# Kernel tuning notes

Hardware: AMD Instinct MI355X
Metric: run time of the kernel (lower is better)

Reference implementation:

```python
import jax, jax.numpy as jnp
import numpy as np

TEMPERATURE = 0.8
TOP_K = 50
TOP_P = 0.9
REP_PENALTY = 1.2
NEG_INF = -1000000000.0


def setup_inputs() -> dict:
    key = jax.random.key(0)
    k1, k2 = jax.random.split(key)
    B, S, V, L = 64, 8, 50257, 2048
    logits = jax.random.normal(k1, (B, S, V), dtype=jnp.float32)
    input_ids = jax.random.randint(k2, (B, L), 0, V, dtype=jnp.int64)
    return {"logits": logits, "input_ids": input_ids}


def _modify_logits(logits, input_ids):
    B, S, V = logits.shape
    # temperature scale
    x = logits / TEMPERATURE
    # top-k: keep values >= k-th largest (ties negligible for random floats)
    kth = jax.lax.top_k(x, TOP_K)[0][..., -1:]  # [B,S,1]
    x = jnp.where(x >= kth, x, NEG_INF)
    # top-p nucleus filtering
    order = jnp.argsort(-x, axis=-1)                       # descending order indices
    sorted_logits = jnp.take_along_axis(x, order, axis=-1)
    cum = jnp.cumsum(jax.nn.softmax(sorted_logits, axis=-1), axis=-1)
    remove = cum > TOP_P
    # shift right by one; always keep the top token
    remove = jnp.concatenate([jnp.zeros_like(remove[..., :1]), remove[..., :-1]], axis=-1)
    inv = jnp.argsort(order, axis=-1)                      # inverse permutation
    remove_orig = jnp.take_along_axis(remove, inv, axis=-1)
    x = jnp.where(remove_orig, NEG_INF, x)
    # repetition penalty on last position only, for tokens present in history
    present = jnp.zeros((B, V), dtype=bool).at[
        jnp.arange(B)[:, None], input_ids
    ].set(True)
    last = x[:, -1, :]
    penalized = jnp.where(last < 0, last * REP_PENALTY, last / REP_PENALTY)
    last = jnp.where(present, penalized, last)
    return x.at[:, -1, :].set(last)


def reference(logits, input_ids):
    return _modify_logits(logits, input_ids)
```

## Files before the change

kernel.cpp:

```cpp
#include <hip/hip_runtime.h>
#include <stdint.h>

#define V 50257
#define B_ 64
#define S_ 8
#define ROWS (B_ * S_)
#define L_ 2048
#define NEG_INF -1000000000.0f
#define PEN_NEG (-1200000000.0f)
#define MASK_WORDS_PER_B 1571
#define TOTAL (ROWS * V)
#define NVEC (TOTAL / 4)
#define TOP_CAP 64
#define TRAW 2.8f
#define GBLK_F4 1571
#define GBLOCKS_G ((NVEC + GBLK_F4 - 1) / GBLK_F4)
#define GCAP_BLK 64
#define CAPROW 512
#define NPRESW ((GBLK_F4 * 4 + 31) / 32)

#define WS_BCNT    0
#define WS_GCAND   16384
#define WS_NEED    (WS_GCAND + (size_t)GBLOCKS_G * GCAP_BLK * 8)
#define WS_ROWPARAM 0
#define WS_MASK     8192

__device__ __forceinline__ unsigned fkey(float f) {
    unsigned u = __float_as_uint(f);
    return (u & 0x80000000u) ? ~u : (u | 0x80000000u);
}

__device__ __forceinline__ int blockReduceSum256(int v, int tid, int* s4) {
#pragma unroll
    for (int off = 32; off; off >>= 1) v += __shfl_down(v, off);
    __syncthreads();
    if ((tid & 63) == 0) s4[tid >> 6] = v;
    __syncthreads();
    return s4[0] + s4[1] + s4[2] + s4[3];
}


__global__ __launch_bounds__(256) void prep_kernel(const float4* __restrict__ in4,
                                                   const int* __restrict__ ids,
                                                   float4* __restrict__ out4,
                                                   uint2* __restrict__ gcand,
                                                   unsigned* __restrict__ bcnt) {
    const int blk = blockIdx.x;
    const int tid = threadIdx.x;
    const int start = blk * GBLK_F4;
    const int end = min(start + GBLK_F4, NVEC);
    const unsigned baseE = (unsigned)start << 2;
    const unsigned endE = (unsigned)end << 2;

    __shared__ unsigned pres[NPRESW];
    __shared__ uint2 buf[GCAP_BLK];
    __shared__ int lcnt;

    for (int w = tid; w < NPRESW; w += 256) pres[w] = 0u;
    if (tid == 0) lcnt = 0;
    {
        unsigned r0 = baseE / (unsigned)V, r1 = (endE - 1u) / (unsigned)V;
        unsigned rl = ((r0 & 7u) == 7u) ? r0 : (((r1 & 7u) == 7u) ? r1 : 0xFFFFFFFFu);
        if (rl != 0xFFFFFFFFu) {
            __syncthreads();
            const int* bp = ids + (rl >> 3) * L_;
            unsigned rowBase = rl * (unsigned)V;
#pragma unroll
            for (int k = 0; k < L_ / 256; ++k) {
                unsigned ge = rowBase + (unsigned)bp[k * 256 + tid];
                if (ge >= baseE && ge < endE) {
                    unsigned off = ge - baseE;
                    atomicOr(&pres[off >> 5], 1u << (off & 31));
                }
            }
        }
    }
    __syncthreads();

    float4 va0 = in4[min(start + tid,            NVEC - 1)];
    float4 va1 = in4[min(start + tid + 256,      NVEC - 1)];
    float4 va2 = in4[min(start + tid + 2 * 256,  NVEC - 1)];
    float4 va3 = in4[min(start + tid + 3 * 256,  NVEC - 1)];
    float4 va4 = in4[min(start + tid + 4 * 256,  NVEC - 1)];
    float4 va5 = in4[min(start + tid + 5 * 256,  NVEC - 1)];
    float4 va6 = in4[min(start + tid + 6 * 256,  NVEC - 1)];
    __builtin_amdgcn_sched_barrier(0);
    float4 va[7] = {va0, va1, va2, va3, va4, va5, va6};
#pragma unroll
    for (int k = 0; k < 7; ++k) {
        int i = start + tid + k * 256;
        if (i < end) {
            float4 a = va[k];
            unsigned e = (unsigned)i << 2;
            if (a.x >= TRAW) { int p = atomicAdd(&lcnt, 1); if (p < GCAP_BLK) buf[p] = make_uint2(e,      __float_as_uint(a.x)); }
            if (a.y >= TRAW) { int p = atomicAdd(&lcnt, 1); if (p < GCAP_BLK) buf[p] = make_uint2(e + 1u, __float_as_uint(a.y)); }
            if (a.z >= TRAW) { int p = atomicAdd(&lcnt, 1); if (p < GCAP_BLK) buf[p] = make_uint2(e + 2u, __float_as_uint(a.z)); }
            if (a.w >= TRAW) { int p = atomicAdd(&lcnt, 1); if (p < GCAP_BLK) buf[p] = make_uint2(e + 3u, __float_as_uint(a.w)); }
            unsigned off = e - baseE;
            unsigned pw = pres[off >> 5] >> (off & 31u);
            float4 bg;
            bg.x = (pw & 1u) ? PEN_NEG : NEG_INF;
            bg.y = (pw & 2u) ? PEN_NEG : NEG_INF;
            bg.z = (pw & 4u) ? PEN_NEG : NEG_INF;
            bg.w = (pw & 8u) ? PEN_NEG : NEG_INF;
            out4[i] = bg;
        }
    }

    __syncthreads();
    if (tid == 0) bcnt[blk] = (unsigned)lcnt;
    int take = min(lcnt, GCAP_BLK);
    for (int j = tid; j < take; j += 256) gcand[(size_t)blk * GCAP_BLK + j] = buf[j];
}


__global__ __launch_bounds__(256) void select_kernel(const float* __restrict__ logits,
                                                     const int* __restrict__ ids,
                                                     const uint2* __restrict__ gcand,
                                                     const unsigned* __restrict__ bcnt,
                                                     float* __restrict__ out) {
    const int row = blockIdx.x;
    const int tid = threadIdx.x;
    __shared__ float cX[CAPROW];
    __shared__ unsigned cR[CAPROW];
    __shared__ int cI[CAPROW];
    __shared__ float sVal[TOP_CAP];
    __shared__ int sIdx[TOP_CAP];
    __shared__ double sExp[TOP_CAP];
    __shared__ unsigned presRow[MASK_WORDS_PER_B];
    __shared__ int s_c, s_M, s_bad, s_ti;
    __shared__ float s_t;
    __shared__ int s_red[4];

    const float* rp = logits + (size_t)row * V;
    const unsigned e0 = (unsigned)row * (unsigned)V;
    if (tid == 0) { s_c = 0; s_bad = 0; }
    __syncthreads();

    {
        const int b0 = (int)((e0 >> 2) / GBLK_F4);
        const int b1 = (int)(((e0 + V - 1) >> 2) / GBLK_F4);
        for (int blk = b0; blk <= b1; ++blk) {
            unsigned c = bcnt[blk];
            if (c > GCAP_BLK && tid == 0) s_bad = 1;
            int take = min((int)c, GCAP_BLK);
            for (int j = tid; j < take; j += 256) {
                uint2 u = gcand[(size_t)blk * GCAP_BLK + j];
                if (u.x / (unsigned)V == (unsigned)row) {
                    int p = atomicAdd(&s_c, 1);
                    if (p < CAPROW) {
                        cR[p] = u.y;
                        cX[p] = __uint_as_float(u.y) / 0.8f;
                        cI[p] = (int)(u.x - e0);
                    }
                }
            }
        }
    }
    __syncthreads();
    int cnt = s_c;
    if (s_bad || cnt < 50 || cnt > CAPROW) {
        unsigned lo = 0u, hi = 0xFFFFFFFFu;
        while (lo < hi) {
            unsigned mid = lo + ((hi - lo) >> 1) + 1u;
            int c = 0;
            for (int j = tid; j < V; j += 256) c += (int)(fkey(rp[j]) >= mid);
            c = blockReduceSum256(c, tid, s_red);
            if (c >= 50) lo = mid; else hi = mid - 1u;
        }
        unsigned gl = (lo > 2u) ? lo - 2u : 0u;
        __syncthreads();
        if (tid == 0) s_c = 0;
        __syncthreads();
        for (int j = tid; j < V; j += 256) {
            float v = rp[j];
            if (fkey(v) >= gl) {
                int p = atomicAdd(&s_c, 1);
                if (p < CAPROW) { cR[p] = __float_as_uint(v); cX[p] = v / 0.8f; cI[p] = j; }
            }
        }
        __syncthreads();
        cnt = min(s_c, CAPROW);
    }

    if (tid < TOP_CAP) { sVal[tid] = -3.4e38f; sIdx[tid] = 0x7FFFFFFF; }
    __syncthreads();

    {
        float v0 = -3.4e38f, v1 = -3.4e38f;
        int i0 = 0x7FFFFFFF, i1 = 0x7FFFFFFF;
        if (tid < cnt) { v0 = cX[tid]; i0 = cI[tid]; }
        if (tid + 256 < cnt) { v1 = cX[tid + 256]; i1 = cI[tid + 256]; }
        int r0 = 0, r1 = 0;
        for (int j = 0; j < cnt; ++j) {
            float w = cX[j];
            int wi = cI[j];
            r0 += (w > v0) || (w == v0 && wi < i0);
            r1 += (w > v1) || (w == v1 && wi < i1);
        }
        if (tid < cnt && r0 < TOP_CAP) { sVal[r0] = v0; sIdx[r0] = i0; }
        if (tid + 256 < cnt && r1 < TOP_CAP) { sVal[r1] = v1; sIdx[r1] = i1; }
    }
    __syncthreads();

    if (tid == 0) {
        float kth = sVal[49];
        int M = 50;
        while (M < TOP_CAP && sVal[M] == kth) ++M;
        s_M = M;
    }
    __syncthreads();
    int M = s_M;
    if (tid < M) sExp[tid] = exp((double)sVal[tid] - (double)sVal[0]);
    __syncthreads();
    if (tid == 0) {
        double denom = 0.0;
        for (int i = 0; i < M; ++i) denom += sExp[i];
        double cum = 0.0;
        int J = M - 1;
        for (int i = 0; i < M; ++i) {
            cum += sExp[i] / denom;
            if (cum > 0.9) { J = i; break; }
        }
        s_t = sVal[J];
        s_ti = sIdx[J];
    }

    if ((row & 7) == 7) {
        __syncthreads();
        for (int w = tid; w < MASK_WORDS_PER_B; w += 256) presRow[w] = 0u;
        __syncthreads();
        const int* bp = ids + (row >> 3) * L_;
#pragma unroll
        for (int k = 0; k < L_ / 256; ++k) {
            int t = bp[k * 256 + tid];
            atomicOr(&presRow[t >> 5], 1u << (t & 31));
        }
    }
    __syncthreads();

    float t = s_t;
    int tie = s_ti;
    float* orow = out + (size_t)row * V;
    const bool pen = (row & 7) == 7;
    for (int j = tid; j < cnt; j += 256) {
        float x = cX[j];
        int tok = cI[j];
        bool keep = (x > t) || (x == t && tok <= tie);
        if (keep) {
            float oo = x;
            if (pen && ((presRow[tok >> 5] >> (tok & 31)) & 1u))
                oo = (oo < 0.0f) ? oo * 1.2f : oo * (1.0f / 1.2f);
            orow[tok] = oo;
        }
    }
}

#define CAND_CAP 4096
#define RT_THREADS 1024

__global__ __launch_bounds__(256) void mask_only_kernel(const int* __restrict__ ids,
                                                        unsigned* __restrict__ mask) {
    const int tid = threadIdx.x;
    const int b = blockIdx.x;
    __shared__ unsigned lds[MASK_WORDS_PER_B];
    for (int w = tid; w < MASK_WORDS_PER_B; w += 256) lds[w] = 0u;
    __syncthreads();
    const int* bp = ids + b * L_;
#pragma unroll
    for (int k = 0; k < L_ / 256; ++k) {
        int t = bp[k * 256 + tid];
        atomicOr(&lds[t >> 5], 1u << (t & 31));
    }
    __syncthreads();
    unsigned* mp = mask + b * MASK_WORDS_PER_B;
    for (int w = tid; w < MASK_WORDS_PER_B; w += 256) mp[w] = lds[w];
}

__global__ __launch_bounds__(RT_THREADS, 8) void row_thresh_kernel(
        const float* __restrict__ logits, uint4* __restrict__ rowParam) {
    const int tid = threadIdx.x;
    const int row = blockIdx.x;
    if (row >= ROWS) return;
    const float* rp = logits + (size_t)row * V;

    __shared__ float candV[CAND_CAP];
    __shared__ int   candI[CAND_CAP];
    __shared__ float sVal[TOP_CAP];
    __shared__ int   sIdx[TOP_CAP];
    __shared__ double sExp[TOP_CAP];
    __shared__ int s_cnt, s_M;
    __shared__ int s_red[RT_THREADS / 64];

    const unsigned mis = (unsigned)(((size_t)row * (size_t)V) & 3u);
    const int a0 = (int)((4u - mis) & 3u);
    const int nv = (V - a0) >> 2;
    const int tailStart = a0 + (nv << 2);
    const float4* vp = reinterpret_cast<const float4*>(rp + a0);

    float TR = 2.4f;
    int cnt = 0;
    for (int attempt = 0; attempt < 12; ++attempt) {
        if (tid == 0) s_cnt = 0;
        __syncthreads();
        for (int base = tid; base < nv; base += 4 * RT_THREADS) {
            int i1 = base + RT_THREADS, i2 = base + 2 * RT_THREADS, i3 = base + 3 * RT_THREADS;
            float4 a = vp[base];
            float4 b = vp[i1 < nv ? i1 : nv - 1];
            float4 c = vp[i2 < nv ? i2 : nv - 1];
            float4 d = vp[i3 < nv ? i3 : nv - 1];
            float va[16] = {a.x, a.y, a.z, a.w, b.x, b.y, b.z, b.w,
                            c.x, c.y, c.z, c.w, d.x, d.y, d.z, d.w};
            int ib[4] = {base, i1, i2, i3};
            bool ok[4] = {true, i1 < nv, i2 < nv, i3 < nv};
#pragma unroll
            for (int q = 0; q < 4; ++q) {
                if (!ok[q]) continue;
#pragma unroll
                for (int cc = 0; cc < 4; ++cc) {
                    float v = va[q * 4 + cc];
                    if (v >= TR) {
                        int p = atomicAdd(&s_cnt, 1);
                        if (p < CAND_CAP) { candV[p] = v / 0.8f; candI[p] = a0 + (ib[q] << 2) + cc; }
                    }
                }
            }
        }
        if (tid < a0) {
            float v = rp[tid];
            if (v >= TR) {
                int p = atomicAdd(&s_cnt, 1);
                if (p < CAND_CAP) { candV[p] = v / 0.8f; candI[p] = tid; }
            }
        }
        if (tid < V - tailStart) {
            float v = rp[tailStart + tid];
            if (v >= TR) {
                int p = atomicAdd(&s_cnt, 1);
                if (p < CAND_CAP) { candV[p] = v / 0.8f; candI[p] = tailStart + tid; }
            }
        }
        __syncthreads();
        cnt = s_cnt;
        if (cnt >= 50 && cnt <= CAND_CAP) break;
        if (cnt < 50) TR -= 1.2f; else TR += 1.2f;
        __syncthreads();
    }
    if (cnt > CAND_CAP) cnt = CAND_CAP;

    if (tid < TOP_CAP) { sVal[tid] = -3.4e38f; sIdx[tid] = 0x7FFFFFFF; }
    __syncthreads();

    {
        float v0 = (tid < cnt) ? candV[tid] : -3.4e38f;
        int i0 = (tid < cnt) ? candI[tid] : 0x7FFFFFFF;
        float v1 = (tid + RT_THREADS < cnt) ? candV[tid + RT_THREADS] : -3.4e38f;
        int i1 = (tid + RT_THREADS < cnt) ? candI[tid + RT_THREADS] : 0x7FFFFFFF;
        float v2 = (tid + 2 * RT_THREADS < cnt) ? candV[tid + 2 * RT_THREADS] : -3.4e38f;
        int i2 = (tid + 2 * RT_THREADS < cnt) ? candI[tid + 2 * RT_THREADS] : 0x7FFFFFFF;
        float v3 = (tid + 3 * RT_THREADS < cnt) ? candV[tid + 3 * RT_THREADS] : -3.4e38f;
        int i3 = (tid + 3 * RT_THREADS < cnt) ? candI[tid + 3 * RT_THREADS] : 0x7FFFFFFF;
        int r0 = 0, r1 = 0, r2 = 0, r3 = 0;
        for (int j = 0; j < cnt; ++j) {
            float w = candV[j];
            int wi = candI[j];
            r0 += (w > v0) || (w == v0 && wi < i0);
            r1 += (w > v1) || (w == v1 && wi < i1);
            r2 += (w > v2) || (w == v2 && wi < i2);
            r3 += (w > v3) || (w == v3 && wi < i3);
        }
        if (tid < cnt && r0 < TOP_CAP) { sVal[r0] = v0; sIdx[r0] = i0; }
        if (tid + RT_THREADS < cnt && r1 < TOP_CAP) { sVal[r1] = v1; sIdx[r1] = i1; }
        if (tid + 2 * RT_THREADS < cnt && r2 < TOP_CAP) { sVal[r2] = v2; sIdx[r2] = i2; }
        if (tid + 3 * RT_THREADS < cnt && r3 < TOP_CAP) { sVal[r3] = v3; sIdx[r3] = i3; }
    }
    __syncthreads();

    if (tid == 0) {
        float kth = sVal[49];
        int M = 50;
        while (M < TOP_CAP && sVal[M] == kth) ++M;
        s_M = M;
    }
    __syncthreads();
    int M = s_M;
    if (tid < M) sExp[tid] = exp((double)sVal[tid] - (double)sVal[0]);
    __syncthreads();

    if (tid == 0) {
        double denom = 0.0;
#pragma unroll 1
        for (int i = 0; i < M; ++i) denom += sExp[i];
        double cum = 0.0;
        int J = M - 1;
#pragma unroll 1
        for (int i = 0; i < M; ++i) {
            cum += sExp[i] / denom;
            if (cum > 0.9) { J = i; break; }
        }
        float t = sVal[J];
        float w = t * 0.8f;
        unsigned wb = __float_as_uint(w);
        unsigned lo = 0xFFFFFFFFu, hi = 0u;
        for (int d = -4; d <= 4; ++d) {
            unsigned ub = wb + (unsigned)d;
            if (__uint_as_float(ub) / 0.8f == t) { if (ub < lo) lo = ub; if (ub > hi) hi = ub; }
        }
        rowParam[row] = make_uint4(lo, hi, (unsigned)sIdx[J], 0u);
    }
}

__global__ __launch_bounds__(256) void apply_kernel(const float4* __restrict__ in4,
                                                    const uint4* __restrict__ rowParam,
                                                    const unsigned* __restrict__ mask,
                                                    float4* __restrict__ out4) {
    int gid = blockIdx.x * 256 + threadIdx.x;
    int i0 = gid << 1;
    if (i0 >= NVEC) return;
    float4 a = in4[i0];
    float4 b = in4[i0 + 1];
    unsigned e = (unsigned)i0 << 2;
    unsigned row = e / (unsigned)V;
    unsigned tok0 = e - row * (unsigned)V;
    uint4 p0 = rowParam[row];
    bool crosses = (tok0 + 7u >= (unsigned)V);
    uint4 p1 = crosses ? rowParam[row + 1] : p0;
    float xs[8] = {a.x, a.y, a.z, a.w, b.x, b.y, b.z, b.w};
    float o[8];
#pragma unroll
    for (int c = 0; c < 8; ++c) {
        unsigned tok = tok0 + (unsigned)c;
        unsigned r = row;
        uint4 pp = p0;
        if (tok >= (unsigned)V) { tok -= (unsigned)V; r = row + 1u; pp = p1; }
        float v = xs[c];
        float vlo = __uint_as_float(pp.x);
        float vhi = __uint_as_float(pp.y);
        bool keep = (v > vhi) || (v >= vlo && tok <= pp.z);
        float oo = keep ? v * 1.25f : NEG_INF;
        if ((r & 7u) == 7u) {
            unsigned w = mask[(r >> 3) * MASK_WORDS_PER_B + (tok >> 5)];
            if ((w >> (tok & 31u)) & 1u) oo = (oo < 0.0f) ? oo * 1.2f : oo * (1.0f / 1.2f);
        }
        o[c] = oo;
    }
    out4[i0] = make_float4(o[0], o[1], o[2], o[3]);
    out4[i0 + 1] = make_float4(o[4], o[5], o[6], o[7]);
}

extern "C" void kernel_launch(void* const* d_in, const int* in_sizes, int n_in,
                              void* d_out, int out_size, void* d_ws, size_t ws_size,
                              hipStream_t stream) {
    const float* logits = (const float*)d_in[0];
    const int* ids = (const int*)d_in[1];
    float* out = (float*)d_out;

    if (ws_size >= WS_NEED) {
        unsigned* bcnt = (unsigned*)((char*)d_ws + WS_BCNT);
        uint2* gcand = (uint2*)((char*)d_ws + WS_GCAND);
        prep_kernel<<<GBLOCKS_G, 256, 0, stream>>>((const float4*)logits, ids, (float4*)out,
                                                   gcand, bcnt);
        select_kernel<<<ROWS, 256, 0, stream>>>(logits, ids, gcand, bcnt, out);
    } else {
        uint4* rowParam = (uint4*)((char*)d_ws + WS_ROWPARAM);
        unsigned* mask = (unsigned*)((char*)d_ws + WS_MASK);
        mask_only_kernel<<<B_, 256, 0, stream>>>(ids, mask);
        row_thresh_kernel<<<ROWS, RT_THREADS, 0, stream>>>(logits, rowParam);
        apply_kernel<<<(NVEC / 2 + 255) / 256, 256, 0, stream>>>((const float4*)logits, rowParam,
                                                                 mask, (float4*)out);
    }
}
```

Measured before the change: 61.21 us.

## Drop presence mask from prep kernel and buffer candidates per thread

```diff
diff --git a/kernel.cpp b/kernel.cpp
--- a/kernel.cpp
+++ b/kernel.cpp
@@ -17,7 +17,6 @@
 #define GBLOCKS_G ((NVEC + GBLK_F4 - 1) / GBLK_F4)
 #define GCAP_BLK 64
 #define CAPROW 512
-#define NPRESW ((GBLK_F4 * 4 + 31) / 32)
 
 #define WS_BCNT    0
 #define WS_GCAND   16384
@@ -41,7 +40,6 @@
 
 
 __global__ __launch_bounds__(256) void prep_kernel(const float4* __restrict__ in4,
-                                                   const int* __restrict__ ids,
                                                    float4* __restrict__ out4,
                                                    uint2* __restrict__ gcand,
                                                    unsigned* __restrict__ bcnt) {
@@ -49,66 +47,50 @@
     const int tid = threadIdx.x;
     const int start = blk * GBLK_F4;
     const int end = min(start + GBLK_F4, NVEC);
-    const unsigned baseE = (unsigned)start << 2;
-    const unsigned endE = (unsigned)end << 2;
-
-    __shared__ unsigned pres[NPRESW];
+
     __shared__ uint2 buf[GCAP_BLK];
-    __shared__ int lcnt;
-
-    for (int w = tid; w < NPRESW; w += 256) pres[w] = 0u;
-    if (tid == 0) lcnt = 0;
-    {
-        unsigned r0 = baseE / (unsigned)V, r1 = (endE - 1u) / (unsigned)V;
-        unsigned rl = ((r0 & 7u) == 7u) ? r0 : (((r1 & 7u) == 7u) ? r1 : 0xFFFFFFFFu);
-        if (rl != 0xFFFFFFFFu) {
-            __syncthreads();
-            const int* bp = ids + (rl >> 3) * L_;
-            unsigned rowBase = rl * (unsigned)V;
-#pragma unroll
-            for (int k = 0; k < L_ / 256; ++k) {
-                unsigned ge = rowBase + (unsigned)bp[k * 256 + tid];
-                if (ge >= baseE && ge < endE) {
-                    unsigned off = ge - baseE;
-                    atomicOr(&pres[off >> 5], 1u << (off & 31));
-                }
-            }
-        }
-    }
-    __syncthreads();
-
-    float4 va0 = in4[min(start + tid,            NVEC - 1)];
-    float4 va1 = in4[min(start + tid + 256,      NVEC - 1)];
-    float4 va2 = in4[min(start + tid + 2 * 256,  NVEC - 1)];
-    float4 va3 = in4[min(start + tid + 3 * 256,  NVEC - 1)];
-    float4 va4 = in4[min(start + tid + 4 * 256,  NVEC - 1)];
-    float4 va5 = in4[min(start + tid + 5 * 256,  NVEC - 1)];
-    float4 va6 = in4[min(start + tid + 6 * 256,  NVEC - 1)];
-    __builtin_amdgcn_sched_barrier(0);
-    float4 va[7] = {va0, va1, va2, va3, va4, va5, va6};
+    __shared__ int lcnt, s_of;
+    if (tid == 0) { lcnt = 0; s_of = 0; }
+    __syncthreads();
+
+    float c0v = 0.f, c1v = 0.f, c2v = 0.f, c3v = 0.f, c4v = 0.f;
+    int c0i = 0, c1i = 0, c2i = 0, c3i = 0, c4i = 0;
+    int nh = 0;
+    const float4 bg = make_float4(NEG_INF, NEG_INF, NEG_INF, NEG_INF);
+
+#define INS(val, ei)                                                          \
+    if ((val) >= TRAW) {                                                      \
+        c4v = c3v; c4i = c3i; c3v = c2v; c3i = c2i; c2v = c1v; c2i = c1i;     \
+        c1v = c0v; c1i = c0i; c0v = (val); c0i = (ei); ++nh;                  \
+    }
+
 #pragma unroll
     for (int k = 0; k < 7; ++k) {
         int i = start + tid + k * 256;
+        float4 a = in4[min(i, NVEC - 1)];
         if (i < end) {
-            float4 a = va[k];
-            unsigned e = (unsigned)i << 2;
-            if (a.x >= TRAW) { int p = atomicAdd(&lcnt, 1); if (p < GCAP_BLK) buf[p] = make_uint2(e,      __float_as_uint(a.x)); }
-            if (a.y >= TRAW) { int p = atomicAdd(&lcnt, 1); if (p < GCAP_BLK) buf[p] = make_uint2(e + 1u, __float_as_uint(a.y)); }
-            if (a.z >= TRAW) { int p = atomicAdd(&lcnt, 1); if (p < GCAP_BLK) buf[p] = make_uint2(e + 2u, __float_as_uint(a.z)); }
-            if (a.w >= TRAW) { int p = atomicAdd(&lcnt, 1); if (p < GCAP_BLK) buf[p] = make_uint2(e + 3u, __float_as_uint(a.w)); }
-            unsigned off = e - baseE;
-            unsigned pw = pres[off >> 5] >> (off & 31u);
-            float4 bg;
-            bg.x = (pw & 1u) ? PEN_NEG : NEG_INF;
-            bg.y = (pw & 2u) ? PEN_NEG : NEG_INF;
-            bg.z = (pw & 4u) ? PEN_NEG : NEG_INF;
-            bg.w = (pw & 8u) ? PEN_NEG : NEG_INF;
             out4[i] = bg;
-        }
-    }
-
-    __syncthreads();
-    if (tid == 0) bcnt[blk] = (unsigned)lcnt;
+            int e = i << 2;
+            INS(a.x, e)
+            INS(a.y, e + 1)
+            INS(a.z, e + 2)
+            INS(a.w, e + 3)
+        }
+    }
+#undef INS
+
+    if (nh > 0) {
+        int m = nh > 5 ? 5 : nh;
+        if (nh > 5) s_of = 1;
+        int base = atomicAdd(&lcnt, m);
+        if (m >= 1 && base + 0 < GCAP_BLK) buf[base + 0] = make_uint2((unsigned)c0i, __float_as_uint(c0v));
+        if (m >= 2 && base + 1 < GCAP_BLK) buf[base + 1] = make_uint2((unsigned)c1i, __float_as_uint(c1v));
+        if (m >= 3 && base + 2 < GCAP_BLK) buf[base + 2] = make_uint2((unsigned)c2i, __float_as_uint(c2v));
+        if (m >= 4 && base + 3 < GCAP_BLK) buf[base + 3] = make_uint2((unsigned)c3i, __float_as_uint(c3v));
+        if (m >= 5 && base + 4 < GCAP_BLK) buf[base + 4] = make_uint2((unsigned)c4i, __float_as_uint(c4v));
+    }
+    __syncthreads();
+    if (tid == 0) bcnt[blk] = s_of ? 1000000u : (unsigned)lcnt;
     int take = min(lcnt, GCAP_BLK);
     for (int j = tid; j < take; j += 256) gcand[(size_t)blk * GCAP_BLK + j] = buf[j];
 }
@@ -226,7 +208,10 @@
         s_ti = sIdx[J];
     }
 
-    if ((row & 7) == 7) {
+    float* orow = out + (size_t)row * V;
+    const bool pen = (row & 7) == 7;
+
+    if (pen) {
         __syncthreads();
         for (int w = tid; w < MASK_WORDS_PER_B; w += 256) presRow[w] = 0u;
         __syncthreads();
@@ -235,14 +220,13 @@
         for (int k = 0; k < L_ / 256; ++k) {
             int t = bp[k * 256 + tid];
             atomicOr(&presRow[t >> 5], 1u << (t & 31));
+            orow[t] = PEN_NEG;
         }
     }
     __syncthreads();
 
     float t = s_t;
     int tie = s_ti;
-    float* orow = out + (size_t)row * V;
-    const bool pen = (row & 7) == 7;
     for (int j = tid; j < cnt; j += 256) {
         float x = cX[j];
         int tok = cI[j];
@@ -458,7 +442,7 @@
     if (ws_size >= WS_NEED) {
         unsigned* bcnt = (unsigned*)((char*)d_ws + WS_BCNT);
         uint2* gcand = (uint2*)((char*)d_ws + WS_GCAND);
-        prep_kernel<<<GBLOCKS_G, 256, 0, stream>>>((const float4*)logits, ids, (float4*)out,
+        prep_kernel<<<GBLOCKS_G, 256, 0, stream>>>((const float4*)logits, (float4*)out,
                                                    gcand, bcnt);
         select_kernel<<<ROWS, 256, 0, stream>>>(logits, ids, gcand, bcnt, out);
     } else {
```

Measured after the change: 61.96 us. No clear change (+1.2%).

## Split prep into wave-level pipelined gather kernel and separate background-fill kernel

Applied to the files above, without the earlier changes.

```diff
diff --git a/kernel.cpp b/kernel.cpp
--- a/kernel.cpp
+++ b/kernel.cpp
@@ -13,15 +13,20 @@
 #define NVEC (TOTAL / 4)
 #define TOP_CAP 64
 #define TRAW 2.8f
-#define GBLK_F4 1571
-#define GBLOCKS_G ((NVEC + GBLK_F4 - 1) / GBLK_F4)
-#define GCAP_BLK 64
+#define WCHUNK_F4 448
+#define ELEMS_PER_CHUNK (WCHUNK_F4 * 4)
+#define NCHUNKS ((NVEC + WCHUNK_F4 - 1) / WCHUNK_F4)
+#define NWAVES_PHYS (NCHUNKS / 4)
+#define GW_BLOCKS ((NWAVES_PHYS + 3) / 4)
+#define WCAP 32
 #define CAPROW 512
-#define NPRESW ((GBLK_F4 * 4 + 31) / 32)
-
-#define WS_BCNT    0
-#define WS_GCAND   16384
-#define WS_NEED    (WS_GCAND + (size_t)GBLOCKS_G * GCAP_BLK * 8)
+#define BG_F4 2048
+#define BG_BLOCKS ((NVEC + BG_F4 - 1) / BG_F4)
+#define BG_PRESW (BG_F4 * 4 / 32)
+
+#define WS_WCNT    0
+#define WS_GCAND   65536
+#define WS_NEED    (WS_GCAND + (size_t)NCHUNKS * WCAP * 8)
 #define WS_ROWPARAM 0
 #define WS_MASK     8192
 
@@ -40,63 +45,138 @@
 }
 
 
-__global__ __launch_bounds__(256) void prep_kernel(const float4* __restrict__ in4,
-                                                   const int* __restrict__ ids,
-                                                   float4* __restrict__ out4,
-                                                   uint2* __restrict__ gcand,
-                                                   unsigned* __restrict__ bcnt) {
+__global__ __launch_bounds__(256) void gather_kernel(const float4* __restrict__ in4,
+                                                     uint2* __restrict__ gcand,
+                                                     unsigned* __restrict__ wcnt) {
+    const int pw = blockIdx.x * 4 + (threadIdx.x >> 6);
+    if (pw >= NWAVES_PHYS) return;
+    const int lane = threadIdx.x & 63;
+    const int c0 = pw * 4;
+
+    float4 a0, a1, a2, a3, a4, a5, a6;
+    float4 b0, b1, b2, b3, b4, b5, b6;
+
+#define GLD(dst, idx)                                                          \
+    { const float4* _p = in4 + min((idx), NVEC - 1);                           \
+      asm volatile("global_load_dwordx4 %0, %1, off" : "=v"(dst) : "v"(_p)); }
+
+#define ISSUE7(s0, s1, s2, s3, s4, s5, s6, cid)                                \
+    { int _b = (cid) * WCHUNK_F4 + lane;                                       \
+      GLD(s0, _b) GLD(s1, _b + 64) GLD(s2, _b + 128) GLD(s3, _b + 192)         \
+      GLD(s4, _b + 256) GLD(s5, _b + 320) GLD(s6, _b + 384)                    \
+      __builtin_amdgcn_sched_barrier(0); }
+
+#define INSQ(val, ei)                                                          \
+    if ((val) >= TRAW) {                                                       \
+        q7v = q6v; q7i = q6i; q6v = q5v; q6i = q5i; q5v = q4v; q5i = q4i;      \
+        q4v = q3v; q4i = q3i; q3v = q2v; q3i = q2i; q2v = q1v; q2i = q1i;      \
+        q1v = q0v; q1i = q0i; q0v = (val); q0i = (ei); ++nh;                   \
+    }
+
+#define CHUNK4(vv, off_)                                                       \
+    { int _i = _b + (off_);                                                    \
+      if (_i < NVEC) { int _e = _i << 2;                                       \
+        INSQ((vv).x, _e) INSQ((vv).y, _e + 1)                                  \
+        INSQ((vv).z, _e + 2) INSQ((vv).w, _e + 3) } }
+
+#define CONSUME_FLUSH(s0, s1, s2, s3, s4, s5, s6, cid)                         \
+    { float q0v = 0.f, q1v = 0.f, q2v = 0.f, q3v = 0.f;                        \
+      float q4v = 0.f, q5v = 0.f, q6v = 0.f, q7v = 0.f;                        \
+      int q0i = 0, q1i = 0, q2i = 0, q3i = 0;                                  \
+      int q4i = 0, q5i = 0, q6i = 0, q7i = 0;                                  \
+      int nh = 0;                                                              \
+      int _b = (cid) * WCHUNK_F4 + lane;                                       \
+      CHUNK4(s0, 0) CHUNK4(s1, 64) CHUNK4(s2, 128) CHUNK4(s3, 192)             \
+      CHUNK4(s4, 256) CHUNK4(s5, 320) CHUNK4(s6, 384)                          \
+      int m = nh > 8 ? 8 : nh;                                                 \
+      int incl = m, _t;                                                        \
+      _t = __shfl_up(incl, 1);  if (lane >= 1)  incl += _t;                    \
+      _t = __shfl_up(incl, 2);  if (lane >= 2)  incl += _t;                    \
+      _t = __shfl_up(incl, 4);  if (lane >= 4)  incl += _t;                    \
+      _t = __shfl_up(incl, 8);  if (lane >= 8)  incl += _t;                    \
+      _t = __shfl_up(incl, 16); if (lane >= 16) incl += _t;                    \
+      _t = __shfl_up(incl, 32); if (lane >= 32) incl += _t;                    \
+      int excl = incl - m;                                                     \
+      int total = __shfl(incl, 63);                                            \
+      bool of = (total > WCAP) || __any(nh > 8);                               \
+      size_t rb = (size_t)(cid) * WCAP;                                        \
+      if (m >= 1 && excl + 0 < WCAP) gcand[rb + excl + 0] = make_uint2((unsigned)q0i, __float_as_uint(q0v)); \
+      if (m >= 2 && excl + 1 < WCAP) gcand[rb + excl + 1] = make_uint2((unsigned)q1i, __float_as_uint(q1v)); \
+      if (m >= 3 && excl + 2 < WCAP) gcand[rb + excl + 2] = make_uint2((unsigned)q2i, __float_as_uint(q2v)); \
+      if (m >= 4 && excl + 3 < WCAP) gcand[rb + excl + 3] = make_uint2((unsigned)q3i, __float_as_uint(q3v)); \
+      if (m >= 5 && excl + 4 < WCAP) gcand[rb + excl + 4] = make_uint2((unsigned)q4i, __float_as_uint(q4v)); \
+      if (m >= 6 && excl + 5 < WCAP) gcand[rb + excl + 5] = make_uint2((unsigned)q5i, __float_as_uint(q5v)); \
+      if (m >= 7 && excl + 6 < WCAP) gcand[rb + excl + 6] = make_uint2((unsigned)q6i, __float_as_uint(q6v)); \
+      if (m >= 8 && excl + 7 < WCAP) gcand[rb + excl + 7] = make_uint2((unsigned)q7i, __float_as_uint(q7v)); \
+      if (lane == 0) wcnt[cid] = of ? 1000000u : (unsigned)total;              \
+      __builtin_amdgcn_sched_barrier(0); }
+
+    ISSUE7(a0, a1, a2, a3, a4, a5, a6, c0)
+    ISSUE7(b0, b1, b2, b3, b4, b5, b6, c0 + 1)
+    asm volatile("s_waitcnt vmcnt(7)" ::: "memory");
+    __builtin_amdgcn_sched_barrier(0);
+    CONSUME_FLUSH(a0, a1, a2, a3, a4, a5, a6, c0)
+    ISSUE7(a0, a1, a2, a3, a4, a5, a6, c0 + 2)
+    asm volatile("s_waitcnt vmcnt(7)" ::: "memory");
+    __builtin_amdgcn_sched_barrier(0);
+    CONSUME_FLUSH(b0, b1, b2, b3, b4, b5, b6, c0 + 1)
+    ISSUE7(b0, b1, b2, b3, b4, b5, b6, c0 + 3)
+    asm volatile("s_waitcnt vmcnt(7)" ::: "memory");
+    __builtin_amdgcn_sched_barrier(0);
+    CONSUME_FLUSH(a0, a1, a2, a3, a4, a5, a6, c0 + 2)
+    asm volatile("s_waitcnt vmcnt(0)" ::: "memory");
+    __builtin_amdgcn_sched_barrier(0);
+    CONSUME_FLUSH(b0, b1, b2, b3, b4, b5, b6, c0 + 3)
+
+#undef CONSUME_FLUSH
+#undef CHUNK4
+#undef INSQ
+#undef ISSUE7
+#undef GLD
+}
+
+
+__global__ __launch_bounds__(256) void bg_kernel(const int* __restrict__ ids,
+                                                 float4* __restrict__ out4) {
     const int blk = blockIdx.x;
     const int tid = threadIdx.x;
-    const int start = blk * GBLK_F4;
-    const int end = min(start + GBLK_F4, NVEC);
+    const int start = blk * BG_F4;
+    const int end = min(start + BG_F4, NVEC);
     const unsigned baseE = (unsigned)start << 2;
     const unsigned endE = (unsigned)end << 2;
 
-    __shared__ unsigned pres[NPRESW];
-    __shared__ uint2 buf[GCAP_BLK];
-    __shared__ int lcnt;
-
-    for (int w = tid; w < NPRESW; w += 256) pres[w] = 0u;
-    if (tid == 0) lcnt = 0;
-    {
-        unsigned r0 = baseE / (unsigned)V, r1 = (endE - 1u) / (unsigned)V;
-        unsigned rl = ((r0 & 7u) == 7u) ? r0 : (((r1 & 7u) == 7u) ? r1 : 0xFFFFFFFFu);
-        if (rl != 0xFFFFFFFFu) {
-            __syncthreads();
-            const int* bp = ids + (rl >> 3) * L_;
-            unsigned rowBase = rl * (unsigned)V;
-#pragma unroll
-            for (int k = 0; k < L_ / 256; ++k) {
-                unsigned ge = rowBase + (unsigned)bp[k * 256 + tid];
-                if (ge >= baseE && ge < endE) {
-                    unsigned off = ge - baseE;
-                    atomicOr(&pres[off >> 5], 1u << (off & 31));
-                }
-            }
-        }
-    }
-    __syncthreads();
-
-    float4 va0 = in4[min(start + tid,            NVEC - 1)];
-    float4 va1 = in4[min(start + tid + 256,      NVEC - 1)];
-    float4 va2 = in4[min(start + tid + 2 * 256,  NVEC - 1)];
-    float4 va3 = in4[min(start + tid + 3 * 256,  NVEC - 1)];
-    float4 va4 = in4[min(start + tid + 4 * 256,  NVEC - 1)];
-    float4 va5 = in4[min(start + tid + 5 * 256,  NVEC - 1)];
-    float4 va6 = in4[min(start + tid + 6 * 256,  NVEC - 1)];
-    __builtin_amdgcn_sched_barrier(0);
-    float4 va[7] = {va0, va1, va2, va3, va4, va5, va6};
-#pragma unroll
-    for (int k = 0; k < 7; ++k) {
+    __shared__ unsigned pres[BG_PRESW];
+
+    unsigned r0 = baseE / (unsigned)V, r1 = (endE - 1u) / (unsigned)V;
+    unsigned rl = ((r0 & 7u) == 7u) ? r0 : (((r1 & 7u) == 7u) ? r1 : 0xFFFFFFFFu);
+
+    if (rl == 0xFFFFFFFFu) {
+        const float4 bg = make_float4(NEG_INF, NEG_INF, NEG_INF, NEG_INF);
+#pragma unroll
+        for (int k = 0; k < 8; ++k) {
+            int i = start + tid + k * 256;
+            if (i < end) out4[i] = bg;
+        }
+        return;
+    }
+    for (int w = tid; w < BG_PRESW; w += 256) pres[w] = 0u;
+    __syncthreads();
+    const int* bp = ids + (rl >> 3) * L_;
+    unsigned rowBase = rl * (unsigned)V;
+#pragma unroll
+    for (int k = 0; k < L_ / 256; ++k) {
+        unsigned ge = rowBase + (unsigned)bp[k * 256 + tid];
+        if (ge >= baseE && ge < endE) {
+            unsigned off = ge - baseE;
+            atomicOr(&pres[off >> 5], 1u << (off & 31));
+        }
+    }
+    __syncthreads();
+#pragma unroll
+    for (int k = 0; k < 8; ++k) {
         int i = start + tid + k * 256;
         if (i < end) {
-            float4 a = va[k];
-            unsigned e = (unsigned)i << 2;
-            if (a.x >= TRAW) { int p = atomicAdd(&lcnt, 1); if (p < GCAP_BLK) buf[p] = make_uint2(e,      __float_as_uint(a.x)); }
-            if (a.y >= TRAW) { int p = atomicAdd(&lcnt, 1); if (p < GCAP_BLK) buf[p] = make_uint2(e + 1u, __float_as_uint(a.y)); }
-            if (a.z >= TRAW) { int p = atomicAdd(&lcnt, 1); if (p < GCAP_BLK) buf[p] = make_uint2(e + 2u, __float_as_uint(a.z)); }
-            if (a.w >= TRAW) { int p = atomicAdd(&lcnt, 1); if (p < GCAP_BLK) buf[p] = make_uint2(e + 3u, __float_as_uint(a.w)); }
-            unsigned off = e - baseE;
+            unsigned off = ((unsigned)i << 2) - baseE;
             unsigned pw = pres[off >> 5] >> (off & 31u);
             float4 bg;
             bg.x = (pw & 1u) ? PEN_NEG : NEG_INF;
@@ -106,28 +186,23 @@
             out4[i] = bg;
         }
     }
-
-    __syncthreads();
-    if (tid == 0) bcnt[blk] = (unsigned)lcnt;
-    int take = min(lcnt, GCAP_BLK);
-    for (int j = tid; j < take; j += 256) gcand[(size_t)blk * GCAP_BLK + j] = buf[j];
 }
 
 
 __global__ __launch_bounds__(256) void select_kernel(const float* __restrict__ logits,
                                                      const int* __restrict__ ids,
                                                      const uint2* __restrict__ gcand,
-                                                     const unsigned* __restrict__ bcnt,
+                                                     const unsigned* __restrict__ wcnt,
                                                      float* __restrict__ out) {
     const int row = blockIdx.x;
     const int tid = threadIdx.x;
     __shared__ float cX[CAPROW];
-    __shared__ unsigned cR[CAPROW];
     __shared__ int cI[CAPROW];
     __shared__ float sVal[TOP_CAP];
     __shared__ int sIdx[TOP_CAP];
     __shared__ double sExp[TOP_CAP];
     __shared__ unsigned presRow[MASK_WORDS_PER_B];
+    __shared__ unsigned s_wc[40];
     __shared__ int s_c, s_M, s_bad, s_ti;
     __shared__ float s_t;
     __shared__ int s_red[4];
@@ -138,18 +213,22 @@
     __syncthreads();
 
     {
-        const int b0 = (int)((e0 >> 2) / GBLK_F4);
-        const int b1 = (int)(((e0 + V - 1) >> 2) / GBLK_F4);
-        for (int blk = b0; blk <= b1; ++blk) {
-            unsigned c = bcnt[blk];
-            if (c > GCAP_BLK && tid == 0) s_bad = 1;
-            int take = min((int)c, GCAP_BLK);
-            for (int j = tid; j < take; j += 256) {
-                uint2 u = gcand[(size_t)blk * GCAP_BLK + j];
+        const int r0 = (int)(e0 / (unsigned)ELEMS_PER_CHUNK);
+        const int r1 = (int)((e0 + V - 1) / (unsigned)ELEMS_PER_CHUNK);
+        const int nr = r1 - r0 + 1;
+        if (tid < nr) s_wc[tid] = wcnt[r0 + tid];
+        __syncthreads();
+        const int nslots = nr * WCAP;
+        for (int j = tid; j < nslots; j += 256) {
+            int r = j >> 5;
+            int sl = j & 31;
+            unsigned c = s_wc[r];
+            if (c > (unsigned)WCAP) { s_bad = 1; c = WCAP; }
+            if (sl < (int)c) {
+                uint2 u = gcand[(size_t)(r0 + r) * WCAP + sl];
                 if (u.x / (unsigned)V == (unsigned)row) {
                     int p = atomicAdd(&s_c, 1);
                     if (p < CAPROW) {
-                        cR[p] = u.y;
                         cX[p] = __uint_as_float(u.y) / 0.8f;
                         cI[p] = (int)(u.x - e0);
                     }
@@ -176,7 +255,7 @@
             float v = rp[j];
             if (fkey(v) >= gl) {
                 int p = atomicAdd(&s_c, 1);
-                if (p < CAPROW) { cR[p] = __float_as_uint(v); cX[p] = v / 0.8f; cI[p] = j; }
+                if (p < CAPROW) { cX[p] = v / 0.8f; cI[p] = j; }
             }
         }
         __syncthreads();
@@ -226,7 +305,8 @@
         s_ti = sIdx[J];
     }
 
-    if ((row & 7) == 7) {
+    const bool pen = (row & 7) == 7;
+    if (pen) {
         __syncthreads();
         for (int w = tid; w < MASK_WORDS_PER_B; w += 256) presRow[w] = 0u;
         __syncthreads();
@@ -242,7 +322,6 @@
     float t = s_t;
     int tie = s_ti;
     float* orow = out + (size_t)row * V;
-    const bool pen = (row & 7) == 7;
     for (int j = tid; j < cnt; j += 256) {
         float x = cX[j];
         int tok = cI[j];
@@ -456,11 +535,11 @@
     float* out = (float*)d_out;
 
     if (ws_size >= WS_NEED) {
-        unsigned* bcnt = (unsigned*)((char*)d_ws + WS_BCNT);
+        unsigned* wcnt = (unsigned*)((char*)d_ws + WS_WCNT);
         uint2* gcand = (uint2*)((char*)d_ws + WS_GCAND);
-        prep_kernel<<<GBLOCKS_G, 256, 0, stream>>>((const float4*)logits, ids, (float4*)out,
-                                                   gcand, bcnt);
-        select_kernel<<<ROWS, 256, 0, stream>>>(logits, ids, gcand, bcnt, out);
+        gather_kernel<<<GW_BLOCKS, 256, 0, stream>>>((const float4*)logits, gcand, wcnt);
+        bg_kernel<<<BG_BLOCKS, 256, 0, stream>>>(ids, (float4*)out);
+        select_kernel<<<ROWS, 256, 0, stream>>>(logits, ids, gcand, wcnt, out);
     } else {
         uint4* rowParam = (uint4*)((char*)d_ws + WS_ROWPARAM);
         unsigned* mask = (unsigned*)((char*)d_ws + WS_MASK);
```

Measured after the change: 61.51 us. Within noise of the previous version (+0.5%).
